# Kernel tuning notes

Hardware: AMD Instinct MI355X
Metric: run time of the kernel (lower is better)

The kernel has to match this reference:

```python
import jax, jax.numpy as jnp
import numpy as np

BATCH, SEQ, D_MODEL, K_SIZE = 2, 4096, 2048, 3


def setup_inputs() -> dict:
    key = jax.random.key(0)
    k1, k2, k3, k4 = jax.random.split(key, 4)
    s = 1.0 / np.sqrt(D_MODEL)
    x = jax.random.normal(k1, (BATCH, SEQ, D_MODEL), dtype=jnp.float32)
    w1 = jax.random.normal(k2, (3 * D_MODEL, D_MODEL), dtype=jnp.float32) * s
    w2 = jax.random.normal(k3, (D_MODEL, D_MODEL), dtype=jnp.float32) * s
    conv_w = jax.random.normal(k4, (D_MODEL, 1, K_SIZE), dtype=jnp.float32) * 0.5
    return {"x": x, "w1": w1, "w2": w2, "conv_w": conv_w}


def _causal_depthwise_conv(u, conv_w):
    # u: [B, D, S]; conv_w: [D, 1, K] (torch Conv1d weight layout, groups=D)
    k = conv_w.shape[-1]
    return jax.lax.conv_general_dilated(
        u, conv_w,
        window_strides=(1,),
        padding=[(k - 1, 0)],  # left pad = causal; matches pad=k-1 then [..., :seq_len]
        feature_group_count=u.shape[1],
        dimension_numbers=("NCH", "OIH", "NCH"),
    )


def reference(x, w1, w2, conv_w):
    # x: [B, S, D]
    BCx = jnp.einsum("bsd,ed->bse", x, w1)           # [B, S, 3D]
    Bg, Cg, Xg = jnp.split(BCx, 3, axis=-1)           # each [B, S, D]
    u = (Bg * Xg).transpose(0, 2, 1)                  # [B, D, S]
    conv_out = _causal_depthwise_conv(u, conv_w)      # [B, D, S]
    gated = Cg * conv_out.transpose(0, 2, 1)          # [B, S, D]
    return jnp.einsum("bsd,ed->bse", gated, w2)       # [B, S, D]
```

## Files before the change

### kernel.cpp

```cpp
#include <hip/hip_runtime.h>
#include <stdint.h>

#define BATCH 2
#define SEQ   4096
#define DM    2048
#define MT    (BATCH*SEQ)
#define N1    (3*DM)
#define STRIP 16

typedef __attribute__((ext_vector_type(8))) __bf16 bf16x8;
typedef __attribute__((ext_vector_type(4))) float  f32x4;
typedef __attribute__((ext_vector_type(8))) unsigned short ushort8v;
typedef __attribute__((ext_vector_type(4))) unsigned short ushort4v;

__device__ inline unsigned short f2bf(float f) {
    uint32_t u = __float_as_uint(f);
    u += 0x7FFFu + ((u >> 16) & 1u);
    return (unsigned short)(u >> 16);
}
__device__ inline float bf2f(unsigned short h) {
    return __uint_as_float(((uint32_t)h) << 16);
}

__global__ void cvt_f32_bf16(const float* __restrict__ src,
                             unsigned short* __restrict__ dst, int n) {
    int i = (blockIdx.x * blockDim.x + threadIdx.x) * 4;
    const int stride = gridDim.x * blockDim.x * 4;
    for (; i < n; i += stride) {
        const float4 v = *(const float4*)(src + i);
        ushort4v o;
        o[0] = f2bf(v.x); o[1] = f2bf(v.y); o[2] = f2bf(v.z); o[3] = f2bf(v.w);
        *(ushort4v*)(dst + i) = o;
    }
}

__device__ inline void async_copy16(const void* g, void* l) {
    __builtin_amdgcn_global_load_lds(
        (const __attribute__((address_space(1))) void*)g,
        (__attribute__((address_space(3))) void*)l,
        16, 0, 0);
}


#define MFMA_(d, a, b) d = __builtin_amdgcn_mfma_f32_16x16x32_bf16(a, b, d, 0, 0, 0)

#define M8(K2, NH, AH, BQ) do { \
  MFMA_(acc[(K2)+0][(NH)*2+0], AH[0][0], BQ[0][0]); \
  MFMA_(acc[(K2)+0][(NH)*2+1], AH[0][0], BQ[1][0]); \
  MFMA_(acc[(K2)+1][(NH)*2+0], AH[1][0], BQ[0][0]); \
  MFMA_(acc[(K2)+1][(NH)*2+1], AH[1][0], BQ[1][0]); \
  MFMA_(acc[(K2)+0][(NH)*2+0], AH[0][1], BQ[0][1]); \
  MFMA_(acc[(K2)+0][(NH)*2+1], AH[0][1], BQ[1][1]); \
  MFMA_(acc[(K2)+1][(NH)*2+0], AH[1][1], BQ[0][1]); \
  MFMA_(acc[(K2)+1][(NH)*2+1], AH[1][1], BQ[1][1]); \
} while (0)

template <bool OUT_BF16>
__global__ __launch_bounds__(512)
void gemm256(const unsigned short* __restrict__ A,
             const unsigned short* __restrict__ B,
             void* __restrict__ Cout, int M, int N, int K) {
    __shared__ __attribute__((aligned(16))) char lds[131072];
    const int tid  = threadIdx.x;
    const int wave = tid >> 6;
    const int lane = tid & 63;
    const int wr = wave >> 2, wc = wave & 3;
    const int l16 = lane & 15, lh = lane >> 4;
    const int NT = K >> 6;

    const int nx = gridDim.x;
    int flat = blockIdx.y * nx + blockIdx.x;
    const int cpx = (nx * gridDim.y) >> 3;
    flat = (flat & 7) * cpx + (flat >> 3);
    const int blockN = (flat % nx) << 8;
    const int blockM = (flat / nx) << 8;

    const int swze = ((((lane & 7) << 4) ^ ((lane >> 3) << 4)) >> 1);
    const int sr   = (wave << 3) + (lane >> 3);
    const unsigned short* Ab = A + (size_t)blockM * K;
    const unsigned short* Bb = B + (size_t)blockN * K;
    const size_t a00 = (size_t)(sr      ) * K + swze;
    const size_t a01 = (size_t)(sr +  64) * K + swze;
    const size_t a10 = (size_t)(sr + 128) * K + swze;
    const size_t a11 = (size_t)(sr + 192) * K + swze;
    const int bsr = ((wave >> 2) << 6) + ((wave & 3) << 3) + (lane >> 3);
    const size_t b00 = (size_t)(bsr      ) * K + swze;
    const size_t b01 = (size_t)(bsr + 128) * K + swze;
    const size_t b10 = (size_t)(bsr +  32) * K + swze;
    const size_t b11 = (size_t)(bsr + 160) * K + swze;
    const int ldsw = wave << 10;

#define STG_A(BUF, U, K0) do { \
    async_copy16(Ab + a##U##0 + (K0), lds + (BUF) + (U)*16384 + ldsw); \
    async_copy16(Ab + a##U##1 + (K0), lds + (BUF) + (U)*16384 + 8192 + ldsw); } while (0)
#define STG_B(BUF, NH, K0) do { \
    async_copy16(Bb + b##NH##0 + (K0), lds + (BUF) + 32768 + (NH)*16384 + ldsw); \
    async_copy16(Bb + b##NH##1 + (K0), lds + (BUF) + 32768 + (NH)*16384 + 8192 + ldsw); } while (0)

    const int rdswz = (l16 & 7) << 4;
    const int ac0 = ((lh << 4)      ) ^ rdswz;
    const int ac1 = (64 + (lh << 4)) ^ rdswz;
    const int aRB = wr * 16384 + l16 * 128;
    const int bRB = 32768 + (wc * 32 + l16) * 128;

#define LDA_(BUF, I, C) (*(const bf16x8*)(lds + (BUF) + aRB + (I)*2048 + (C)))
#define LDB_(BUF, J, C) (*(const bf16x8*)(lds + (BUF) + bRB + ((J)>>1)*16384 + ((J)&1)*2048 + (C)))

#define RD_A(DST, BUF, HI) do { \
    DST[0][0]=LDA_(BUF,2*(HI)  ,ac0); DST[0][1]=LDA_(BUF,2*(HI)  ,ac1); \
    DST[1][0]=LDA_(BUF,2*(HI)+1,ac0); DST[1][1]=LDA_(BUF,2*(HI)+1,ac1); } while (0)
#define RD_B(DST, BUF, NH) do { \
    DST[0][0]=LDB_(BUF,2*(NH)  ,ac0); DST[0][1]=LDB_(BUF,2*(NH)  ,ac1); \
    DST[1][0]=LDB_(BUF,2*(NH)+1,ac0); DST[1][1]=LDB_(BUF,2*(NH)+1,ac1); } while (0)

    f32x4 acc[8][4] = {};
    bf16x8 afP[2][2], afQ[2][2], bq0[2][2], bq1[2][2];

    STG_B(0, 0, 0); STG_B(0, 1, 0); STG_A(0, 0, 0); STG_A(0, 1, 0);
    STG_B(65536, 0, 64); STG_B(65536, 1, 64);
    STG_A(65536, 0, 64); STG_A(65536, 1, 64);
    asm volatile("s_waitcnt vmcnt(8)" ::: "memory");
    __builtin_amdgcn_s_barrier();
    RD_B(bq0, 0, 0);
    RD_A(afP, 0, 0);

#define SP1 __builtin_amdgcn_s_setprio(1)
#define SP0 __builtin_amdgcn_s_setprio(0)

#define ITER(CUR, NXT, T) do { \
     \
    RD_B(bq1, CUR, 1); \
    RD_A(afQ, CUR, 1); \
    SP1; M8(0, 0, afP, bq0); SP0; \
     \
    __builtin_amdgcn_s_barrier(); \
    if ((T) + 2 < NT) STG_B(CUR, 0, ((T)+2)*64); \
    SP1; M8(0, 1, afP, bq1); SP0; \
     \
    RD_A(afP, CUR, 2); \
    SP1; M8(2, 0, afQ, bq0); SP0; \
     \
    __builtin_amdgcn_s_barrier(); \
    if ((T) + 2 < NT) STG_B(CUR, 1, ((T)+2)*64); \
    SP1; M8(2, 1, afQ, bq1); SP0; \
     \
    RD_A(afQ, CUR, 3); \
    SP1; M8(4, 0, afP, bq0); SP0; \
     \
    SP1; M8(4, 1, afP, bq1); SP0; \
    if ((T) + 2 < NT)      { asm volatile("s_waitcnt vmcnt(4)" ::: "memory"); } \
    else if ((T) + 1 < NT) { asm volatile("s_waitcnt vmcnt(0)" ::: "memory"); } \
     \
    __builtin_amdgcn_s_barrier(); \
    if ((T) + 1 < NT) RD_A(afP, NXT, 0); \
    SP1; M8(6, 0, afQ, bq0); SP0; \
     \
    __builtin_amdgcn_s_barrier(); \
    if ((T) + 2 < NT) { STG_A(CUR, 0, ((T)+2)*64); STG_A(CUR, 1, ((T)+2)*64); } \
    if ((T) + 1 < NT) RD_B(bq0, NXT, 0); \
    SP1; M8(6, 1, afQ, bq1); SP0; \
} while (0)

    for (int t = 0; t < NT; t += 2) {
        ITER(0, 65536, t);
        ITER(65536, 0, t + 1);
    }

    const int orow = blockM + wr * 128 + (lh << 2);
    const int ocol = blockN + wc * 64 + l16;
    #pragma unroll
    for (int i = 0; i < 8; ++i) {
        #pragma unroll
        for (int j = 0; j < 4; ++j) {
            #pragma unroll
            for (int r = 0; r < 4; ++r) {
                const int row = orow + i * 16 + r;
                const int col = ocol + j * 16;
                if constexpr (OUT_BF16)
                    ((unsigned short*)Cout)[(size_t)row * N + col] = f2bf(acc[i][j][r]);
                else
                    ((float*)Cout)[(size_t)row * N + col] = acc[i][j][r];
            }
        }
    }
#undef ITER
#undef RD_A
#undef RD_B
#undef LDA_
#undef LDB_
#undef STG_A
#undef STG_B
}

__global__ void conv_gate_kernel(const unsigned short* __restrict__ BCx,
                                 const float* __restrict__ cw,
                                 unsigned short* __restrict__ gated) {
    const int tid = threadIdx.x;
    const int d0  = tid * 8;
    const int nstrips = SEQ / STRIP;
    const int b   = blockIdx.x / nstrips;
    const int s0  = (blockIdx.x % nstrips) * STRIP;

    float w0[8], w1c[8], w2c[8];
    #pragma unroll
    for (int c = 0; c < 8; ++c) {
        w0[c]  = cw[(d0 + c) * 3 + 0];
        w1c[c] = cw[(d0 + c) * 3 + 1];
        w2c[c] = cw[(d0 + c) * 3 + 2];
    }

    float um1[8], um2[8];
    if (s0 > 0) {
        const unsigned short* r2 = BCx + (size_t)(b * SEQ + s0 - 2) * N1;
        const unsigned short* r1 = BCx + (size_t)(b * SEQ + s0 - 1) * N1;
        ushort8v bg2 = *(const ushort8v*)(r2 + d0);
        ushort8v xg2 = *(const ushort8v*)(r2 + 2 * DM + d0);
        ushort8v bg1 = *(const ushort8v*)(r1 + d0);
        ushort8v xg1 = *(const ushort8v*)(r1 + 2 * DM + d0);
        #pragma unroll
        for (int c = 0; c < 8; ++c) {
            um2[c] = bf2f(bg2[c]) * bf2f(xg2[c]);
            um1[c] = bf2f(bg1[c]) * bf2f(xg1[c]);
        }
    } else {
        #pragma unroll
        for (int c = 0; c < 8; ++c) { um2[c] = 0.f; um1[c] = 0.f; }
    }

    for (int s = s0; s < s0 + STRIP; ++s) {
        const size_t m = (size_t)b * SEQ + s;
        const unsigned short* rp = BCx + m * N1;
        ushort8v bg = *(const ushort8v*)(rp + d0);
        ushort8v cg = *(const ushort8v*)(rp + DM + d0);
        ushort8v xg = *(const ushort8v*)(rp + 2 * DM + d0);
        ushort8v og;
        #pragma unroll
        for (int c = 0; c < 8; ++c) {
            const float u    = bf2f(bg[c]) * bf2f(xg[c]);
            const float conv = w0[c] * um2[c] + w1c[c] * um1[c] + w2c[c] * u;
            const float g    = bf2f(cg[c]) * conv;
            um2[c] = um1[c];
            um1[c] = u;
            og[c]  = f2bf(g);
        }
        *(ushort8v*)(gated + m * DM + d0) = og;
    }
}

extern "C" void kernel_launch(void* const* d_in, const int* in_sizes, int n_in,
                              void* d_out, int out_size, void* d_ws, size_t ws_size,
                              hipStream_t stream) {
    const float* x   = (const float*)d_in[0];
    const float* w1  = (const float*)d_in[1];
    const float* w2  = (const float*)d_in[2];
    const float* cw  = (const float*)d_in[3];
    float* out = (float*)d_out;

    char* ws = (char*)d_ws;
    unsigned short* x_bf   = (unsigned short*)ws;
    unsigned short* w1_bf  = x_bf  + (size_t)MT * DM;
    unsigned short* w2_bf  = w1_bf + (size_t)N1 * DM;
    unsigned short* bcx_bf = w2_bf + (size_t)DM * DM;
    unsigned short* g_bf   = bcx_bf + (size_t)MT * N1;

    cvt_f32_bf16<<<2048, 256, 0, stream>>>(x,  x_bf,  MT * DM);
    cvt_f32_bf16<<<1024, 256, 0, stream>>>(w1, w1_bf, N1 * DM);
    cvt_f32_bf16<<<512,  256, 0, stream>>>(w2, w2_bf, DM * DM);

    gemm256<true><<<dim3(N1 / 256, MT / 256), 512, 0, stream>>>(
        x_bf, w1_bf, bcx_bf, MT, N1, DM);

    conv_gate_kernel<<<BATCH * (SEQ / STRIP), 256, 0, stream>>>(bcx_bf, cw, g_bf);

    gemm256<false><<<dim3(DM / 256, MT / 256), 512, 0, stream>>>(
        g_bf, w2_bf, out, MT, DM, DM);
}
```

Baseline: 306.4 us.

## Merge fp32-to-bf16 conversions into one launch and split A-tile prefetch

```diff
diff --git a/kernel.cpp b/kernel.cpp
--- a/kernel.cpp
+++ b/kernel.cpp
@@ -22,12 +22,20 @@
     return __uint_as_float(((uint32_t)h) << 16);
 }
 
-__global__ void cvt_f32_bf16(const float* __restrict__ src,
-                             unsigned short* __restrict__ dst, int n) {
-    int i = (blockIdx.x * blockDim.x + threadIdx.x) * 4;
-    const int stride = gridDim.x * blockDim.x * 4;
-    for (; i < n; i += stride) {
-        const float4 v = *(const float4*)(src + i);
+__global__ void cvt_all_bf16(const float* __restrict__ s0, int n0,
+                             const float* __restrict__ s1, int n1,
+                             const float* __restrict__ s2, int n2,
+                             unsigned short* __restrict__ dst) {
+    const int total = (n0 + n1 + n2) >> 2;
+    const int stride = gridDim.x * blockDim.x;
+    for (int q = blockIdx.x * blockDim.x + threadIdx.x; q < total; q += stride) {
+        const int i = q << 2;
+        const float* src;
+        int off;
+        if (i < n0)            { src = s0; off = i; }
+        else if (i < n0 + n1)  { src = s1; off = i - n0; }
+        else                   { src = s2; off = i - n0 - n1; }
+        const float4 v = *(const float4*)(src + off);
         ushort4v o;
         o[0] = f2bf(v.x); o[1] = f2bf(v.y); o[2] = f2bf(v.z); o[3] = f2bf(v.w);
         *(ushort4v*)(dst + i) = o;
@@ -40,7 +48,6 @@
         (__attribute__((address_space(3))) void*)l,
         16, 0, 0);
 }
-
 
 #define MFMA_(d, a, b) d = __builtin_amdgcn_mfma_f32_16x16x32_bf16(a, b, d, 0, 0, 0)
 
@@ -56,7 +63,7 @@
 } while (0)
 
 template <bool OUT_BF16>
-__global__ __launch_bounds__(512)
+__global__ __launch_bounds__(512, 1)
 void gemm256(const unsigned short* __restrict__ A,
              const unsigned short* __restrict__ B,
              void* __restrict__ Cout, int M, int N, int K) {
@@ -144,11 +151,13 @@
     if ((T) + 2 < NT) STG_B(CUR, 1, ((T)+2)*64); \
     SP1; M8(2, 1, afQ, bq1); SP0; \
      \
+    __builtin_amdgcn_s_barrier(); \
+    if ((T) + 2 < NT) STG_A(CUR, 0, ((T)+2)*64); \
     RD_A(afQ, CUR, 3); \
     SP1; M8(4, 0, afP, bq0); SP0; \
      \
     SP1; M8(4, 1, afP, bq1); SP0; \
-    if ((T) + 2 < NT)      { asm volatile("s_waitcnt vmcnt(4)" ::: "memory"); } \
+    if ((T) + 2 < NT)      { asm volatile("s_waitcnt vmcnt(6)" ::: "memory"); } \
     else if ((T) + 1 < NT) { asm volatile("s_waitcnt vmcnt(0)" ::: "memory"); } \
      \
     __builtin_amdgcn_s_barrier(); \
@@ -156,7 +165,7 @@
     SP1; M8(6, 0, afQ, bq0); SP0; \
      \
     __builtin_amdgcn_s_barrier(); \
-    if ((T) + 2 < NT) { STG_A(CUR, 0, ((T)+2)*64); STG_A(CUR, 1, ((T)+2)*64); } \
+    if ((T) + 2 < NT) STG_A(CUR, 1, ((T)+2)*64); \
     if ((T) + 1 < NT) RD_B(bq0, NXT, 0); \
     SP1; M8(6, 1, afQ, bq1); SP0; \
 } while (0)
@@ -263,9 +272,9 @@
     unsigned short* bcx_bf = w2_bf + (size_t)DM * DM;
     unsigned short* g_bf   = bcx_bf + (size_t)MT * N1;
 
-    cvt_f32_bf16<<<2048, 256, 0, stream>>>(x,  x_bf,  MT * DM);
-    cvt_f32_bf16<<<1024, 256, 0, stream>>>(w1, w1_bf, N1 * DM);
-    cvt_f32_bf16<<<512,  256, 0, stream>>>(w2, w2_bf, DM * DM);
+    cvt_all_bf16<<<3072, 256, 0, stream>>>(x,  MT * DM,
+                                           w1, N1 * DM,
+                                           w2, DM * DM, x_bf);
 
     gemm256<true><<<dim3(N1 / 256, MT / 256), 512, 0, stream>>>(
         x_bf, w1_bf, bcx_bf, MT, N1, DM);
```

After: 299.4 us. -2.3%, faster.
